# Optimization experiments

Measured on AMD Instinct MI355X. Metric: run time of the kernel, lower is better.

The kernel has to match this reference:

```python
import jax, jax.numpy as jnp
import numpy as np

B, S, E = 8, 2048, 512
H = 8          # attention heads (and also number of sampling points)
P = 8          # deformable sampling points per token
Dh = E // H


def setup_inputs() -> dict:
    key = jax.random.key(0)
    ks = jax.random.split(key, 9)
    scale = 0.02
    return {
        "q": jax.random.normal(ks[0], (B, S, E), jnp.float32),
        "k": jax.random.normal(ks[1], (B, S, E), jnp.float32),
        "v": jax.random.normal(ks[2], (B, S, E), jnp.float32),
        "offset_w": jax.random.normal(ks[3], (2 * P, E), jnp.float32) * scale,
        "offset_b": jnp.zeros((2 * P,), jnp.float32),
        "in_proj_w": jax.random.normal(ks[4], (3 * E, E), jnp.float32) * scale,
        "in_proj_b": jnp.zeros((3 * E,), jnp.float32),
        "out_w": jax.random.normal(ks[5], (E, E), jnp.float32) * scale,
        "out_b": jnp.zeros((E,), jnp.float32),
    }


def reference(q, k, v, offset_w, offset_b, in_proj_w, in_proj_b, out_w, out_b):
    b, s, e = q.shape
    # learned offsets: [B,S,P,2]; only component 0 is used as a temporal offset
    offsets = (q @ offset_w.T + offset_b).reshape(b, s, P, 2)
    t = jnp.arange(s, dtype=q.dtype)[None, :, None]                # [1,S,1]
    # index = clamp(int(t + off0), 0, S-1); python int() truncates toward zero
    idx = jnp.clip(jnp.trunc(t + offsets[..., 0]).astype(jnp.int32), 0, s - 1)  # [B,S,P]
    # gather sampled K/V: [B,S,P,E]
    sk = jnp.take_along_axis(k[:, :, None, :], idx[..., None], axis=1)
    sv = jnp.take_along_axis(v[:, :, None, :], idx[..., None], axis=1)

    # nn.MultiheadAttention with query len 1 per token, kv len P, batch = B*S
    wq, wk, wv = in_proj_w[:e], in_proj_w[e:2 * e], in_proj_w[2 * e:]
    bq, bk, bv = in_proj_b[:e], in_proj_b[e:2 * e], in_proj_b[2 * e:]
    n = b * s
    qp = (q.reshape(n, e) @ wq.T + bq).reshape(n, H, Dh)            # [N,H,Dh]
    kp = (sk.reshape(n, P, e) @ wk.T + bk).reshape(n, P, H, Dh)     # [N,P,H,Dh]
    vp = (sv.reshape(n, P, e) @ wv.T + bv).reshape(n, P, H, Dh)
    scores = jnp.einsum('nhd,nphd->nhp', qp, kp) / np.sqrt(Dh)      # [N,H,P]
    attn = jax.nn.softmax(scores, axis=-1)
    ctx = jnp.einsum('nhp,nphd->nhd', attn, vp).reshape(n, e)       # [N,E]
    out = ctx @ out_w.T + out_b
    return out.reshape(b, s, e)
```

## Files before the change

### kernel.cpp

```cpp
#include <hip/hip_runtime.h>

#define S_LEN 2048
#define E_DIM 512
#define NTOK  16384

typedef __bf16 bf16x8_t __attribute__((ext_vector_type(8)));
typedef float f32x4_t __attribute__((ext_vector_type(4)));
typedef unsigned short u16x8_t __attribute__((ext_vector_type(8)));

__device__ __forceinline__ float bf2f(unsigned short h) {
  return __uint_as_float(((unsigned)h) << 16);
}
__device__ __forceinline__ u16x8_t cvt8n(float4 a, float4 b) {
  bf16x8_t t;
  t[0] = (__bf16)a.x; t[1] = (__bf16)a.y; t[2] = (__bf16)a.z; t[3] = (__bf16)a.w;
  t[4] = (__bf16)b.x; t[5] = (__bf16)b.y; t[6] = (__bf16)b.z; t[7] = (__bf16)b.w;
  union { bf16x8_t h; u16x8_t u; } cv; cv.h = t; return cv.u;
}
__device__ __forceinline__ void gload16(const void* g, void* l) {
  __builtin_amdgcn_global_load_lds(
      (const __attribute__((address_space(1))) unsigned int*)g,
      (__attribute__((address_space(3))) unsigned int*)l, 16, 0, 0);
}

__global__ __launch_bounds__(256)
void offsets_kernel(const float* __restrict__ q, const float* __restrict__ ow,
                    const float* __restrict__ ob, int* __restrict__ idx,
                    unsigned short* __restrict__ Qbf)
{
  const int wid  = threadIdx.x >> 6;
  const int lane = threadIdx.x & 63;
  const int n = blockIdx.x * 4 + wid;
  const int s = n & (S_LEN - 1);
  const float* qr = q + (size_t)n * E_DIM + lane * 8;
  const float4 q0 = *(const float4*)qr;
  const float4 q1 = *(const float4*)(qr + 4);
  *(u16x8_t*)(Qbf + (size_t)n * E_DIM + lane * 8) = cvt8n(q0, q1);
  float myoff = 0.f;
  #pragma unroll
  for (int p = 0; p < 8; ++p) {
    const float* wr = ow + (size_t)(2 * p) * E_DIM + lane * 8;
    const float4 w0 = *(const float4*)wr;
    const float4 w1 = *(const float4*)(wr + 4);
    float acc = q0.x*w0.x + q0.y*w0.y + q0.z*w0.z + q0.w*w0.w
              + q1.x*w1.x + q1.y*w1.y + q1.z*w1.z + q1.w*w1.w;
    #pragma unroll
    for (int d = 32; d; d >>= 1) acc += __shfl_xor(acc, d, 64);
    if ((lane & 7) == p) myoff = acc;
  }
  if (lane < 8) {
    float off = myoff + ob[2 * lane];
    float val = (float)s + off;
    int id = (int)truncf(val);
    id = id < 0 ? 0 : (id > S_LEN - 1 ? S_LEN - 1 : id);
    idx[n * 8 + lane] = id;
  }
}

__global__ __launch_bounds__(256)
void cvt_kernel(const float* __restrict__ k, const float* __restrict__ v,
                const float* __restrict__ ipw, const float* __restrict__ ow,
                unsigned short* __restrict__ Kb, unsigned short* __restrict__ Vb,
                unsigned short* __restrict__ Wb, unsigned short* __restrict__ OWb)
{
  const int bid = blockIdx.x;
  const float* src; unsigned short* dst; size_t off;
  if (bid < 4096)       { src = k;   dst = Kb;  off = (size_t)bid * 2048; }
  else if (bid < 8192)  { src = v;   dst = Vb;  off = (size_t)(bid - 4096) * 2048; }
  else if (bid < 8576)  { src = ipw; dst = Wb;  off = (size_t)(bid - 8192) * 2048; }
  else                  { src = ow;  dst = OWb; off = (size_t)(bid - 8576) * 2048; }
  const size_t i = off + (size_t)threadIdx.x * 8;
  const float4 a = *(const float4*)(src + i);
  const float4 b = *(const float4*)(src + i + 4);
  *(u16x8_t*)(dst + i) = cvt8n(a, b);
}

template<int OUT_BF16>
__global__ __launch_bounds__(256, 2)
void gemm_kernel(const unsigned short* __restrict__ A0, const unsigned short* __restrict__ A1,
                 const unsigned short* __restrict__ A2, const unsigned short* __restrict__ W,
                 const float* __restrict__ bias, void* __restrict__ Cout)
{
  __shared__ __align__(16) unsigned short sA[2][128 * 64];
  __shared__ __align__(16) unsigned short sB[2][128 * 64];

  const int z = blockIdx.z;
  const unsigned short* A = (z == 0) ? A0 : ((z == 1) ? A1 : A2);
  const unsigned short* Wz = W + (size_t)z * E_DIM * E_DIM;
  const float* bz = bias + (size_t)z * E_DIM;

  const int t    = threadIdx.x;
  const int lane = t & 63;
  const int wid  = t >> 6;
  const int wm   = wid >> 1;
  const int wn   = wid & 1;
  const size_t m0 = (size_t)blockIdx.x * 128;
  const size_t n0 = (size_t)blockIdx.y * 128;

  const int srow0  = wid * 32;
  const int schunk = (lane & 7) ^ (lane >> 3);
  const unsigned short* gA = A  + (m0 + srow0 + (lane >> 3)) * E_DIM + schunk * 8;
  const unsigned short* gB = Wz + (n0 + srow0 + (lane >> 3)) * E_DIM + schunk * 8;

#define STAGE(buf, k0) do { \
    _Pragma("unroll") \
    for (int i_ = 0; i_ < 4; ++i_) { \
      gload16(gA + (size_t)(i_ * 8) * E_DIM + (k0), &sA[buf][(srow0 + i_ * 8) * 64]); \
      gload16(gB + (size_t)(i_ * 8) * E_DIM + (k0), &sB[buf][(srow0 + i_ * 8) * 64]); \
    } } while (0)

  f32x4_t acc[4][4];
  #pragma unroll
  for (int i = 0; i < 4; ++i)
    #pragma unroll
    for (int j = 0; j < 4; ++j)
      acc[i][j] = (f32x4_t){0.f, 0.f, 0.f, 0.f};

  STAGE(0, 0);
  int cur = 0;
  const int fr = lane & 15;
  const int ck0 = lane >> 4;

  for (int kt = 0; kt < 8; ++kt) {
    __syncthreads();
    if (kt < 7) STAGE(cur ^ 1, (kt + 1) * 64);
    #pragma unroll
    for (int kk = 0; kk < 64; kk += 32) {
      const int ckb = (kk >> 3) + ck0;
      bf16x8_t af[4], bfv[4];
      #pragma unroll
      for (int i = 0; i < 4; ++i) {
        const int ra = wm * 64 + i * 16 + fr;
        af[i] = *(const bf16x8_t*)&sA[cur][ra * 64 + ((ckb ^ (ra & 7)) << 3)];
      }
      #pragma unroll
      for (int j = 0; j < 4; ++j) {
        const int rb = wn * 64 + j * 16 + fr;
        bfv[j] = *(const bf16x8_t*)&sB[cur][rb * 64 + ((ckb ^ (rb & 7)) << 3)];
      }
      #pragma unroll
      for (int i = 0; i < 4; ++i)
        #pragma unroll
        for (int j = 0; j < 4; ++j)
          acc[i][j] = __builtin_amdgcn_mfma_f32_16x16x32_bf16(af[i], bfv[j], acc[i][j], 0, 0, 0);
    }
    cur ^= 1;
  }
#undef STAGE

  unsigned short* Cb = (unsigned short*)Cout + (size_t)z * NTOK * E_DIM;
  float* Cf = (float*)Cout;
  #pragma unroll
  for (int i = 0; i < 4; ++i) {
    const int row = (int)m0 + wm * 64 + i * 16 + (lane >> 4) * 4;
    #pragma unroll
    for (int j = 0; j < 4; ++j) {
      const int col = (int)n0 + wn * 64 + j * 16 + fr;
      const float bv = bz[col];
      #pragma unroll
      for (int r = 0; r < 4; ++r) {
        const float val = acc[i][j][r] + bv;
        if constexpr (OUT_BF16)
          Cb[(size_t)(row + r) * E_DIM + col] = __builtin_bit_cast(unsigned short, (__bf16)val);
        else
          Cf[(size_t)(row + r) * E_DIM + col] = val;
      }
    }
  }
}

__global__ __launch_bounds__(256)
void attn_kernel(const unsigned short* __restrict__ Qp, const unsigned short* __restrict__ Kp,
                 const unsigned short* __restrict__ Vp, const int* __restrict__ idx,
                 unsigned short* __restrict__ ctx)
{
  const int wid  = threadIdx.x >> 6;
  const int lane = threadIdx.x & 63;
  const int n = blockIdx.x * 4 + wid;
  const int b = n >> 11;
  const int h = lane >> 3;
  const int p = lane & 7;

  const int id = idx[n * 8 + p];
  const size_t krow = ((size_t)(b << 11) + id) * E_DIM + h * 64;
  const unsigned short* qb = Qp + (size_t)n * E_DIM + h * 64;

  float sc = 0.f;
  #pragma unroll
  for (int j = 0; j < 8; ++j) {
    u16x8_t qv = *(const u16x8_t*)(qb + j * 8);
    u16x8_t kv = *(const u16x8_t*)(Kp + krow + j * 8);
    #pragma unroll
    for (int e = 0; e < 8; ++e) sc += bf2f(qv[e]) * bf2f(kv[e]);
  }
  sc *= 0.125f;

  float m = sc;
  m = fmaxf(m, __shfl_xor(m, 1, 64));
  m = fmaxf(m, __shfl_xor(m, 2, 64));
  m = fmaxf(m, __shfl_xor(m, 4, 64));
  const float ex = __expf(sc - m);
  float dsum = ex;
  dsum += __shfl_xor(dsum, 1, 64);
  dsum += __shfl_xor(dsum, 2, 64);
  dsum += __shfl_xor(dsum, 4, 64);
  const float attn = ex / dsum;

  const int d0 = p * 8;
  float cacc[8];
  #pragma unroll
  for (int j = 0; j < 8; ++j) cacc[j] = 0.f;
  #pragma unroll
  for (int pp = 0; pp < 8; ++pp) {
    const float ap = __shfl(attn, (lane & 56) + pp, 64);
    const int  idp = __shfl(id,   (lane & 56) + pp, 64);
    const unsigned short* vb = Vp + ((size_t)(b << 11) + idp) * E_DIM + h * 64 + d0;
    u16x8_t vv = *(const u16x8_t*)vb;
    #pragma unroll
    for (int j = 0; j < 8; ++j) cacc[j] += ap * bf2f(vv[j]);
  }
  u16x8_t cc;
  #pragma unroll
  for (int j = 0; j < 8; ++j) cc[j] = __builtin_bit_cast(unsigned short, (__bf16)cacc[j]);
  *(u16x8_t*)(ctx + (size_t)n * E_DIM + h * 64 + d0) = cc;
}

extern "C" void kernel_launch(void* const* d_in, const int* in_sizes, int n_in,
                              void* d_out, int out_size, void* d_ws, size_t ws_size,
                              hipStream_t stream) {
  const float* q        = (const float*)d_in[0];
  const float* k        = (const float*)d_in[1];
  const float* v        = (const float*)d_in[2];
  const float* offset_w = (const float*)d_in[3];
  const float* offset_b = (const float*)d_in[4];
  const float* in_proj_w = (const float*)d_in[5];
  const float* in_proj_b = (const float*)d_in[6];
  const float* out_w    = (const float*)d_in[7];
  const float* out_b    = (const float*)d_in[8];

  char* ws = (char*)d_ws;
  unsigned short* Qbf = (unsigned short*)ws;
  unsigned short* Kbf = Qbf + (size_t)NTOK * E_DIM;
  unsigned short* Vbf = Kbf + (size_t)NTOK * E_DIM;
  unsigned short* Wb  = Vbf + (size_t)NTOK * E_DIM;
  unsigned short* OWb = Wb + (size_t)3 * E_DIM * E_DIM;
  unsigned short* Qp  = OWb + (size_t)E_DIM * E_DIM;
  unsigned short* Kp  = Qp + (size_t)NTOK * E_DIM;
  unsigned short* Vp  = Kp + (size_t)NTOK * E_DIM;
  int* idxb = (int*)(Vp + (size_t)NTOK * E_DIM);
  unsigned short* ctxb = Qbf;

  offsets_kernel<<<NTOK / 4, 256, 0, stream>>>(q, offset_w, offset_b, idxb, Qbf);
  cvt_kernel<<<8704, 256, 0, stream>>>(k, v, in_proj_w, out_w, Kbf, Vbf, Wb, OWb);
  gemm_kernel<1><<<dim3(NTOK / 128, E_DIM / 128, 3), 256, 0, stream>>>(
      Qbf, Kbf, Vbf, Wb, in_proj_b, (void*)Qp);
  attn_kernel<<<NTOK / 4, 256, 0, stream>>>(Qp, Kp, Vp, idxb, ctxb);
  gemm_kernel<0><<<dim3(NTOK / 128, E_DIM / 128, 1), 256, 0, stream>>>(
      ctxb, ctxb, ctxb, OWb, out_b, d_out);
}
```

Before: 105.5 us.

## Fuse fp32-to-bf16 conversion of q/k/v into the projection GEMM A-tile load

The standalone conversion kernel is gone. The input-projection GEMM now reads fp32 q/k/v straight from global memory into registers, converts them to bf16 and writes them into the swizzled LDS tile after the MFMA step, which double-buffers the A operand through registers. Weight conversion is folded into extra blocks of the offsets kernel, so there is one fewer launch. This is meant to remove the round trip of writing and re-reading bf16 copies of the activations. The cost is twice the bytes per A load in the GEMM, plus register-staged loads in place of direct-to-LDS loads, which raises register pressure.

```diff
diff --git a/kernel.cpp b/kernel.cpp
--- a/kernel.cpp
+++ b/kernel.cpp
@@ -3,6 +3,8 @@
 #define S_LEN 2048
 #define E_DIM 512
 #define NTOK  16384
+#define NOFF  4096
+#define NWCVT 512
 
 typedef __bf16 bf16x8_t __attribute__((ext_vector_type(8)));
 typedef float f32x4_t __attribute__((ext_vector_type(4)));
@@ -24,18 +26,30 @@
 }
 
 __global__ __launch_bounds__(256)
-void offsets_kernel(const float* __restrict__ q, const float* __restrict__ ow,
+void offsets_kernel(const float* __restrict__ q, const float* __restrict__ ipw,
+                    const float* __restrict__ outw, const float* __restrict__ ow,
                     const float* __restrict__ ob, int* __restrict__ idx,
-                    unsigned short* __restrict__ Qbf)
+                    unsigned short* __restrict__ Wb, unsigned short* __restrict__ OWb)
 {
+  const int bid = blockIdx.x;
+  if (bid >= NOFF) {
+    const int cb = bid - NOFF;
+    const float* src; unsigned short* dst; size_t base;
+    if (cb < 384) { src = ipw;  dst = Wb;  base = (size_t)cb * 2048; }
+    else          { src = outw; dst = OWb; base = (size_t)(cb - 384) * 2048; }
+    const size_t e = base + (size_t)threadIdx.x * 8;
+    const float4 a = *(const float4*)(src + e);
+    const float4 b = *(const float4*)(src + e + 4);
+    *(u16x8_t*)(dst + e) = cvt8n(a, b);
+    return;
+  }
   const int wid  = threadIdx.x >> 6;
   const int lane = threadIdx.x & 63;
-  const int n = blockIdx.x * 4 + wid;
+  const int n = bid * 4 + wid;
   const int s = n & (S_LEN - 1);
   const float* qr = q + (size_t)n * E_DIM + lane * 8;
   const float4 q0 = *(const float4*)qr;
   const float4 q1 = *(const float4*)(qr + 4);
-  *(u16x8_t*)(Qbf + (size_t)n * E_DIM + lane * 8) = cvt8n(q0, q1);
   float myoff = 0.f;
   #pragma unroll
   for (int p = 0; p < 8; ++p) {
@@ -57,35 +71,19 @@
   }
 }
 
-__global__ __launch_bounds__(256)
-void cvt_kernel(const float* __restrict__ k, const float* __restrict__ v,
-                const float* __restrict__ ipw, const float* __restrict__ ow,
-                unsigned short* __restrict__ Kb, unsigned short* __restrict__ Vb,
-                unsigned short* __restrict__ Wb, unsigned short* __restrict__ OWb)
-{
-  const int bid = blockIdx.x;
-  const float* src; unsigned short* dst; size_t off;
-  if (bid < 4096)       { src = k;   dst = Kb;  off = (size_t)bid * 2048; }
-  else if (bid < 8192)  { src = v;   dst = Vb;  off = (size_t)(bid - 4096) * 2048; }
-  else if (bid < 8576)  { src = ipw; dst = Wb;  off = (size_t)(bid - 8192) * 2048; }
-  else                  { src = ow;  dst = OWb; off = (size_t)(bid - 8576) * 2048; }
-  const size_t i = off + (size_t)threadIdx.x * 8;
-  const float4 a = *(const float4*)(src + i);
-  const float4 b = *(const float4*)(src + i + 4);
-  *(u16x8_t*)(dst + i) = cvt8n(a, b);
-}
-
-template<int OUT_BF16>
+template<int A_FP32, int OUT_BF16>
 __global__ __launch_bounds__(256, 2)
-void gemm_kernel(const unsigned short* __restrict__ A0, const unsigned short* __restrict__ A1,
-                 const unsigned short* __restrict__ A2, const unsigned short* __restrict__ W,
+void gemm_kernel(const void* __restrict__ A0v, const void* __restrict__ A1v,
+                 const void* __restrict__ A2v, const unsigned short* __restrict__ W,
                  const float* __restrict__ bias, void* __restrict__ Cout)
 {
   __shared__ __align__(16) unsigned short sA[2][128 * 64];
   __shared__ __align__(16) unsigned short sB[2][128 * 64];
 
   const int z = blockIdx.z;
-  const unsigned short* A = (z == 0) ? A0 : ((z == 1) ? A1 : A2);
+  const void* Av = (z == 0) ? A0v : ((z == 1) ? A1v : A2v);
+  const float* Af = (const float*)Av;
+  const unsigned short* Ab = (const unsigned short*)Av;
   const unsigned short* Wz = W + (size_t)z * E_DIM * E_DIM;
   const float* bz = bias + (size_t)z * E_DIM;
 
@@ -99,14 +97,36 @@
 
   const int srow0  = wid * 32;
   const int schunk = (lane & 7) ^ (lane >> 3);
-  const unsigned short* gA = A  + (m0 + srow0 + (lane >> 3)) * E_DIM + schunk * 8;
   const unsigned short* gB = Wz + (n0 + srow0 + (lane >> 3)) * E_DIM + schunk * 8;
-
-#define STAGE(buf, k0) do { \
-    _Pragma("unroll") \
-    for (int i_ = 0; i_ < 4; ++i_) { \
+  const unsigned short* gA = Ab + (m0 + srow0 + (lane >> 3)) * E_DIM + schunk * 8;
+
+  const int arow  = t >> 1;
+  const int cbase = (t & 1) * 4;
+  const float* gAf = Af + (m0 + arow) * E_DIM + cbase * 8;
+  float4 a_r[8];
+
+#define B_STAGE(buf, k0) do { \
+    _Pragma("unroll") \
+    for (int i_ = 0; i_ < 4; ++i_) \
+      gload16(gB + (size_t)(i_ * 8) * E_DIM + (k0), &sB[buf][(srow0 + i_ * 8) * 64]); \
+  } while (0)
+#define AB_STAGE(buf, k0) do { \
+    _Pragma("unroll") \
+    for (int i_ = 0; i_ < 4; ++i_) \
       gload16(gA + (size_t)(i_ * 8) * E_DIM + (k0), &sA[buf][(srow0 + i_ * 8) * 64]); \
-      gload16(gB + (size_t)(i_ * 8) * E_DIM + (k0), &sB[buf][(srow0 + i_ * 8) * 64]); \
+  } while (0)
+#define A_LOAD(k0) do { \
+    _Pragma("unroll") \
+    for (int c_ = 0; c_ < 4; ++c_) { \
+      const float* ap = gAf + (k0) + c_ * 8; \
+      a_r[2 * c_]     = *(const float4*)ap; \
+      a_r[2 * c_ + 1] = *(const float4*)(ap + 4); \
+    } } while (0)
+#define A_WRITE(buf) do { \
+    _Pragma("unroll") \
+    for (int c_ = 0; c_ < 4; ++c_) { \
+      const int c = cbase + c_; \
+      *(u16x8_t*)&sA[buf][arow * 64 + ((c ^ (arow & 7)) << 3)] = cvt8n(a_r[2 * c_], a_r[2 * c_ + 1]); \
     } } while (0)
 
   f32x4_t acc[4][4];
@@ -116,14 +136,18 @@
     for (int j = 0; j < 4; ++j)
       acc[i][j] = (f32x4_t){0.f, 0.f, 0.f, 0.f};
 
-  STAGE(0, 0);
+  if constexpr (A_FP32) { A_LOAD(0); B_STAGE(0, 0); A_WRITE(0); }
+  else                  { AB_STAGE(0, 0); B_STAGE(0, 0); }
   int cur = 0;
   const int fr = lane & 15;
   const int ck0 = lane >> 4;
 
   for (int kt = 0; kt < 8; ++kt) {
     __syncthreads();
-    if (kt < 7) STAGE(cur ^ 1, (kt + 1) * 64);
+    if (kt < 7) {
+      if constexpr (A_FP32) { A_LOAD((kt + 1) * 64); B_STAGE(cur ^ 1, (kt + 1) * 64); }
+      else                  { AB_STAGE(cur ^ 1, (kt + 1) * 64); B_STAGE(cur ^ 1, (kt + 1) * 64); }
+    }
     #pragma unroll
     for (int kk = 0; kk < 64; kk += 32) {
       const int ckb = (kk >> 3) + ck0;
@@ -144,9 +168,15 @@
         for (int j = 0; j < 4; ++j)
           acc[i][j] = __builtin_amdgcn_mfma_f32_16x16x32_bf16(af[i], bfv[j], acc[i][j], 0, 0, 0);
     }
+    if (kt < 7) {
+      if constexpr (A_FP32) A_WRITE(cur ^ 1);
+    }
     cur ^= 1;
   }
-#undef STAGE
+#undef B_STAGE
+#undef AB_STAGE
+#undef A_LOAD
+#undef A_WRITE
 
   unsigned short* Cb = (unsigned short*)Cout + (size_t)z * NTOK * E_DIM;
   float* Cf = (float*)Cout;
@@ -239,22 +269,19 @@
   const float* out_b    = (const float*)d_in[8];
 
   char* ws = (char*)d_ws;
-  unsigned short* Qbf = (unsigned short*)ws;
-  unsigned short* Kbf = Qbf + (size_t)NTOK * E_DIM;
-  unsigned short* Vbf = Kbf + (size_t)NTOK * E_DIM;
-  unsigned short* Wb  = Vbf + (size_t)NTOK * E_DIM;
-  unsigned short* OWb = Wb + (size_t)3 * E_DIM * E_DIM;
-  unsigned short* Qp  = OWb + (size_t)E_DIM * E_DIM;
-  unsigned short* Kp  = Qp + (size_t)NTOK * E_DIM;
-  unsigned short* Vp  = Kp + (size_t)NTOK * E_DIM;
-  int* idxb = (int*)(Vp + (size_t)NTOK * E_DIM);
-  unsigned short* ctxb = Qbf;
-
-  offsets_kernel<<<NTOK / 4, 256, 0, stream>>>(q, offset_w, offset_b, idxb, Qbf);
-  cvt_kernel<<<8704, 256, 0, stream>>>(k, v, in_proj_w, out_w, Kbf, Vbf, Wb, OWb);
-  gemm_kernel<1><<<dim3(NTOK / 128, E_DIM / 128, 3), 256, 0, stream>>>(
-      Qbf, Kbf, Vbf, Wb, in_proj_b, (void*)Qp);
+  unsigned short* Wb   = (unsigned short*)ws;
+  unsigned short* OWb  = Wb + (size_t)3 * E_DIM * E_DIM;
+  unsigned short* Qp   = OWb + (size_t)E_DIM * E_DIM;
+  unsigned short* Kp   = Qp + (size_t)NTOK * E_DIM;
+  unsigned short* Vp   = Kp + (size_t)NTOK * E_DIM;
+  unsigned short* ctxb = Vp + (size_t)NTOK * E_DIM;
+  int* idxb = (int*)(ctxb + (size_t)NTOK * E_DIM);
+
+  offsets_kernel<<<NOFF + NWCVT, 256, 0, stream>>>(q, in_proj_w, out_w, offset_w, offset_b,
+                                                   idxb, Wb, OWb);
+  gemm_kernel<1, 1><<<dim3(NTOK / 128, E_DIM / 128, 3), 256, 0, stream>>>(
+      q, k, v, Wb, in_proj_b, (void*)Qp);
   attn_kernel<<<NTOK / 4, 256, 0, stream>>>(Qp, Kp, Vp, idxb, ctxb);
-  gemm_kernel<0><<<dim3(NTOK / 128, E_DIM / 128, 1), 256, 0, stream>>>(
+  gemm_kernel<0, 0><<<dim3(NTOK / 128, E_DIM / 128, 1), 256, 0, stream>>>(
       ctxb, ctxb, ctxb, OWb, out_b, d_out);
 }
```

Result: slower. 128.0 us (+21.3%).
